# Optimization experiments

Measured on AMD Instinct MI355X. Metric: run time of the kernel, lower is better.

## Reference

```python
import jax, jax.numpy as jnp
import numpy as np

PROJ_DIM = 128
CLASS_NUM = 7
QUEUE_SIZE = 150
TEMP = 0.5
EPS = 1e-8


def _l2norm(x):
    # torch F.normalize(dim=1) with eps clamp
    n = jnp.linalg.norm(x, axis=1, keepdims=True)
    return x / jnp.maximum(n, 1e-12)


def setup_inputs() -> dict:
    key = jax.random.key(0)
    k1, k2, k3, k4 = jax.random.split(key, 4)
    B = 65536
    activation = jax.random.normal(k1, (B, PROJ_DIM), dtype=jnp.float32)
    ema_activation = jax.random.normal(k2, (B, PROJ_DIM), dtype=jnp.float32)
    pseudo_label = jax.random.normal(k3, (B, CLASS_NUM), dtype=jnp.float32)
    queue_list = jax.random.normal(k4, (QUEUE_SIZE * CLASS_NUM, PROJ_DIM), dtype=jnp.float32)
    queue_list = _l2norm(queue_list)  # buffer is row-normalized at init
    return {
        "activation": activation,
        "ema_activation": ema_activation,
        "pseudo_label": pseudo_label,
        "queue_list": queue_list,
    }


def reference(activation, ema_activation, pseudo_label, queue_list):
    f = _l2norm(activation)          # [B, D]
    ema_f = _l2norm(ema_activation)  # [B, D]
    label = jnp.argmax(pseudo_label, axis=1)  # [B]

    # positive pair term: exp(<f_i, ema_f_i>/T)
    l_pos = jnp.exp(jnp.sum(f * ema_f, axis=1) / TEMP)  # [B]

    # similarities against the (snapshotted) queue: [B, C*Qs]
    sim = jnp.exp(jnp.einsum("bd,qd->bq", f, queue_list) / TEMP)

    # denominator = l_pos + pos_sum + neg_sum = l_pos + total_sum over queue
    denom = l_pos + jnp.sum(sim, axis=1)  # [B]

    # which queue rows belong to each sample's pseudo-class
    row_class = jnp.arange(CLASS_NUM * QUEUE_SIZE) // QUEUE_SIZE  # [C*Qs]
    pos_mask = (row_class[None, :] == label[:, None])             # [B, C*Qs]

    # -log(contrast) terms: the ema term plus the QUEUE_SIZE positive terms
    term0 = -jnp.log(l_pos / denom + EPS)                          # [B]
    term1 = -jnp.log(sim / denom[:, None] + EPS)                   # [B, C*Qs]
    pos_terms = jnp.sum(jnp.where(pos_mask, term1, 0.0), axis=1)   # [B]

    per_sample = (term0 + pos_terms) / (QUEUE_SIZE + 1)
    return jnp.mean(per_sample)
```

## Files before the change

kernel.cpp:

```cpp
#include <hip/hip_runtime.h>
#include <stdint.h>

#define CLASS_NUM 7
#define QROWS 1050
#define QPAD  1152
#define NPAD  102
#define NGRP  72
#define GPW   18
#define QSUM_OFF (QPAD * 128)
#define PART_OFF 151552
#define NBLK  1024
#define C2L 2.8853900817779268f
#define USCALE 0x7F7F7F7F

typedef float f32x4 __attribute__((ext_vector_type(4)));
typedef int   i32x8 __attribute__((ext_vector_type(8)));

__device__ __forceinline__ float fexp2(float x) { return __builtin_amdgcn_exp2f(x); }

__device__ __forceinline__ unsigned pk8(float a, float b, float c, float d) {
  int v = __builtin_amdgcn_cvt_pk_fp8_f32(a, b, 0, false);
  v = __builtin_amdgcn_cvt_pk_fp8_f32(c, d, v, true);
  return (unsigned)v;
}

__global__ __launch_bounds__(256) void prep_q8(
    const float* __restrict__ queue, char* __restrict__ ws)
{
  const int b = blockIdx.x, tid = threadIdx.x;
  if (b < NGRP) {
    const int g = b;
    const int lane = tid >> 2, k = tid & 3;
    const int row = g * 16 + (lane & 15);
    const int col = (lane >> 4) * 32 + k * 8;
    uint2 u = {0u, 0u};
    if (row < QROWS) {
      const float4 v0 = *(const float4*)(queue + row * 128 + col);
      const float4 v1 = *(const float4*)(queue + row * 128 + col + 4);
      u.x = pk8(v0.x, v0.y, v0.z, v0.w);
      u.y = pk8(v1.x, v1.y, v1.z, v1.w);
    }
    *(uint2*)(ws + (size_t)g * 2048 + tid * 8) = u;
  } else if (tid < 128) {
    const int c = b - NGRP, d = tid;
    float s = 0.f;
    const float* p = queue + c * 150 * 128 + d;
#pragma unroll 10
    for (int i = 0; i < 150; ++i) s += p[i * 128];
    ((float*)(ws + QSUM_OFF))[c * 128 + d] = s;
  }
}

__global__ __launch_bounds__(256, 2) void pgc_stream(
    const float* __restrict__ act, const float* __restrict__ ema,
    const float* __restrict__ plab, char* __restrict__ ws)
{
  __shared__ __align__(16) char aT[8192];
  __shared__ float s_lpos[64], s_pd[64];
  __shared__ float dnp[4][64];

  const int tid = threadIdx.x, lane = tid & 63, wave = tid >> 6;
  const int lo = lane & 15, hi = lane >> 4;

  {
    const int r = tid >> 2, j4 = tid & 3;
    const long grow = (long)blockIdx.x * 64 + r;
    const float* ap = act + grow * 128 + j4 * 32;
    const float* ep = ema + grow * 128 + j4 * 32;

    float pv0 = plab[grow * CLASS_NUM + j4];
    float pv1 = (j4 + 4 < CLASS_NUM) ? plab[grow * CLASS_NUM + j4 + 4] : -3.4e38f;
    f32x4 a4[8], e4[8];
#pragma unroll
    for (int u = 0; u < 8; ++u) a4[u] = *(const f32x4*)(ap + 4 * u);
#pragma unroll
    for (int u = 0; u < 8; ++u) e4[u] = *(const f32x4*)(ep + 4 * u);

    float a2 = 0.f, e2 = 0.f, ae = 0.f;
#pragma unroll
    for (int u = 0; u < 8; ++u) {
      a2 += a4[u].x*a4[u].x + a4[u].y*a4[u].y + a4[u].z*a4[u].z + a4[u].w*a4[u].w;
      e2 += e4[u].x*e4[u].x + e4[u].y*e4[u].y + e4[u].z*e4[u].z + e4[u].w*e4[u].w;
      ae += a4[u].x*e4[u].x + a4[u].y*e4[u].y + a4[u].z*e4[u].z + a4[u].w*e4[u].w;
    }
#pragma unroll
    for (int m = 1; m < 4; m <<= 1) {
      a2 += __shfl_xor(a2, m);
      e2 += __shfl_xor(e2, m);
      ae += __shfl_xor(ae, m);
    }
    const float rna = rsqrtf(a2), rne = rsqrtf(e2);

    float pv = pv0; int bi = j4;
    if (pv1 > pv0) { pv = pv1; bi = j4 + 4; }
#pragma unroll
    for (int m = 1; m < 4; m <<= 1) {
      const float ov = __shfl_xor(pv, m);
      const int   oi = __shfl_xor(bi, m);
      if (ov > pv || (ov == pv && oi < bi)) { pv = ov; bi = oi; }
    }

    const float* qs = (const float*)(ws + QSUM_OFF) + bi * 128 + j4 * 32;
    float pdot = 0.f;
#pragma unroll
    for (int u = 0; u < 8; ++u) {
      const float4 qv = *(const float4*)(qs + 4 * u);
      pdot += a4[u].x*qv.x + a4[u].y*qv.y + a4[u].z*qv.z + a4[u].w*qv.w;
    }
#pragma unroll
    for (int m = 1; m < 4; m <<= 1) pdot += __shfl_xor(pdot, m);

    if (j4 == 0) {
      s_lpos[r] = ae * rna * rne * C2L;
      s_pd[r]   = pdot * rna;
    }

    const float sc = rna * C2L;
    const int st = r >> 4, tl = j4 * 16 + (r & 15);
    uint4 w0, w1;
    w0.x = pk8(a4[0].x*sc, a4[0].y*sc, a4[0].z*sc, a4[0].w*sc);
    w0.y = pk8(a4[1].x*sc, a4[1].y*sc, a4[1].z*sc, a4[1].w*sc);
    w0.z = pk8(a4[2].x*sc, a4[2].y*sc, a4[2].z*sc, a4[2].w*sc);
    w0.w = pk8(a4[3].x*sc, a4[3].y*sc, a4[3].z*sc, a4[3].w*sc);
    w1.x = pk8(a4[4].x*sc, a4[4].y*sc, a4[4].z*sc, a4[4].w*sc);
    w1.y = pk8(a4[5].x*sc, a4[5].y*sc, a4[5].z*sc, a4[5].w*sc);
    w1.z = pk8(a4[6].x*sc, a4[6].y*sc, a4[6].z*sc, a4[6].w*sc);
    w1.w = pk8(a4[7].x*sc, a4[7].y*sc, a4[7].z*sc, a4[7].w*sc);
    *(uint4*)(aT + st * 2048 + tl * 32)      = w0;
    *(uint4*)(aT + st * 2048 + tl * 32 + 16) = w1;
  }
  __syncthreads();

  i32x8 sa[4];
#pragma unroll
  for (int s = 0; s < 4; ++s)
    sa[s] = *(const i32x8*)(aT + s * 2048 + lane * 32);

  float dn[4][4] = {{0.f,0.f,0.f,0.f},{0.f,0.f,0.f,0.f},
                    {0.f,0.f,0.f,0.f},{0.f,0.f,0.f,0.f}};
  const f32x4 Z = {0.f, 0.f, 0.f, 0.f};
  const char* qp = ws + (size_t)(wave * GPW) * 2048 + (size_t)lane * 32;

  i32x8 B0, B1, B2;
#define LOADG(X, G)  { X = *(const i32x8*)(qp + (G) * 2048); }
#define COMPG(X)                                                        \
  { _Pragma("unroll")                                                   \
    for (int s = 0; s < 4; ++s) {                                       \
      f32x4 c = __builtin_amdgcn_mfma_scale_f32_16x16x128_f8f6f4(       \
          sa[s], X, Z, 0, 0, 0, USCALE, 0, USCALE);                     \
      _Pragma("unroll")                                                 \
      for (int rg = 0; rg < 4; ++rg) dn[s][rg] += fexp2(c[rg]);         \
    } }

  LOADG(B0, 0)
  LOADG(B1, 1)
  LOADG(B2, 2)
#pragma unroll 1
  for (int g = 0; g < GPW - 3; g += 3) {
    COMPG(B0) LOADG(B0, g + 3)
    COMPG(B1) LOADG(B1, g + 4)
    COMPG(B2) LOADG(B2, g + 5)
  }
  COMPG(B0)
  COMPG(B1)
  COMPG(B2)
#undef LOADG
#undef COMPG

#pragma unroll
  for (int s = 0; s < 4; ++s)
#pragma unroll
    for (int rg = 0; rg < 4; ++rg)
#pragma unroll
      for (int m = 1; m < 16; m <<= 1)
        dn[s][rg] += __shfl_xor(dn[s][rg], m);

  if (lo == 0) {
#pragma unroll
    for (int s = 0; s < 4; ++s)
#pragma unroll
      for (int rg = 0; rg < 4; ++rg)
        dnp[wave][s * 16 + hi * 4 + rg] = dn[s][rg];
  }
  __syncthreads();

  if (tid < 64) {
    const int i = tid;
    const float dtot = dnp[0][i] + dnp[1][i] + dnp[2][i] + dnp[3][i];
    const float lp   = exp2f(s_lpos[i]);
    const float dnf  = lp + dtot - (float)NPAD;
    float loss = -logf(lp / dnf + 1e-8f) + 150.0f * logf(dnf) - 2.0f * s_pd[i];
#pragma unroll
    for (int m = 1; m < 64; m <<= 1) loss += __shfl_xor(loss, m);
    if (tid == 0)
      ((float*)(ws + PART_OFF))[blockIdx.x] = loss;
  }
}

__global__ __launch_bounds__(1024) void finalize(
    const char* __restrict__ ws, float* __restrict__ out)
{
  __shared__ float sred[16];
  const int tid = threadIdx.x;
  float v = ((const float*)(ws + PART_OFF))[tid];
#pragma unroll
  for (int m = 1; m < 64; m <<= 1) v += __shfl_xor(v, m);
  if ((tid & 63) == 0) sred[tid >> 6] = v;
  __syncthreads();
  if (tid < 16) {
    float s = sred[tid];
#pragma unroll
    for (int m = 1; m < 16; m <<= 1) s += __shfl_xor(s, m);
    if (tid == 0) *out = s * (1.0f / (151.0f * 65536.0f));
  }
}

extern "C" void kernel_launch(void* const* d_in, const int* in_sizes, int n_in,
                              void* d_out, int out_size, void* d_ws, size_t ws_size,
                              hipStream_t stream) {
  const float* act   = (const float*)d_in[0];
  const float* ema   = (const float*)d_in[1];
  const float* plab  = (const float*)d_in[2];
  const float* queue = (const float*)d_in[3];
  float* out = (float*)d_out;

  prep_q8<<<dim3(NGRP + CLASS_NUM), dim3(256), 0, stream>>>(queue, (char*)d_ws);

  pgc_stream<<<dim3(NBLK), dim3(256), 0, stream>>>(act, ema, plab, (char*)d_ws);

  finalize<<<dim3(1), dim3(1024), 0, stream>>>((const char*)d_ws, out);
}
```

Before: 38.50 us.

## Stage activation and EMA tiles through LDS with direct global-to-LDS loads

```diff
diff --git a/kernel.cpp b/kernel.cpp
--- a/kernel.cpp
+++ b/kernel.cpp
@@ -55,79 +55,72 @@
     const float* __restrict__ act, const float* __restrict__ ema,
     const float* __restrict__ plab, char* __restrict__ ws)
 {
-  __shared__ __align__(16) char aT[8192];
-  __shared__ float s_lpos[64], s_pd[64];
-  __shared__ float dnp[4][64];
+  __shared__ __align__(16) char smem[75520];
+  char*  stage  = smem;
+  char*  aT     = smem + 65536;
+  int*   s_lab  = (int*)  (smem + 73728);
+  float* s_lpos = (float*)(smem + 73984);
+  float* s_pd   = (float*)(smem + 74240);
+  float (*dnp)[64] = (float(*)[64])(smem + 74496);
 
   const int tid = threadIdx.x, lane = tid & 63, wave = tid >> 6;
   const int lo = lane & 15, hi = lane >> 4;
 
   {
-    const int r = tid >> 2, j4 = tid & 3;
-    const long grow = (long)blockIdx.x * 64 + r;
-    const float* ap = act + grow * 128 + j4 * 32;
-    const float* ep = ema + grow * 128 + j4 * 32;
-
-    float pv0 = plab[grow * CLASS_NUM + j4];
-    float pv1 = (j4 + 4 < CLASS_NUM) ? plab[grow * CLASS_NUM + j4 + 4] : -3.4e38f;
-    f32x4 a4[8], e4[8];
-#pragma unroll
-    for (int u = 0; u < 8; ++u) a4[u] = *(const f32x4*)(ap + 4 * u);
-#pragma unroll
-    for (int u = 0; u < 8; ++u) e4[u] = *(const f32x4*)(ep + 4 * u);
-
-    float a2 = 0.f, e2 = 0.f, ae = 0.f;
-#pragma unroll
-    for (int u = 0; u < 8; ++u) {
-      a2 += a4[u].x*a4[u].x + a4[u].y*a4[u].y + a4[u].z*a4[u].z + a4[u].w*a4[u].w;
-      e2 += e4[u].x*e4[u].x + e4[u].y*e4[u].y + e4[u].z*e4[u].z + e4[u].w*e4[u].w;
-      ae += a4[u].x*e4[u].x + a4[u].y*e4[u].y + a4[u].z*e4[u].z + a4[u].w*e4[u].w;
+    const char* actB = (const char*)(act + (size_t)blockIdx.x * 64 * 128);
+    const char* emaB = (const char*)(ema + (size_t)blockIdx.x * 64 * 128);
+    const char* src = (wave < 2) ? actB + wave * 16384 : emaB + (wave - 2) * 16384;
+    char* dst = stage + wave * 16384;
+#pragma unroll
+    for (int i = 0; i < 16; ++i)
+      __builtin_amdgcn_global_load_lds(
+          (const __attribute__((address_space(1))) void*)(src + i * 1024 + lane * 16),
+          (__attribute__((address_space(3))) void*)(dst + i * 1024), 16, 0, 0);
+  }
+
+  if (tid < 64) {
+    const float* pp = plab + ((size_t)blockIdx.x * 64 + tid) * CLASS_NUM;
+    float best = pp[0]; int bi = 0;
+#pragma unroll
+    for (int c = 1; c < CLASS_NUM; ++c) {
+      const float v = pp[c];
+      if (v > best) { best = v; bi = c; }
     }
-#pragma unroll
-    for (int m = 1; m < 4; m <<= 1) {
-      a2 += __shfl_xor(a2, m);
-      e2 += __shfl_xor(e2, m);
-      ae += __shfl_xor(ae, m);
+    s_lab[tid] = bi;
+  }
+  __syncthreads();
+
+  {
+    const int b5 = tid & 31;
+    const int h  = tid >> 5;
+#pragma unroll
+    for (int k = 0; k < 8; ++k) {
+      const int row = h + k * 8;
+      const f32x4 a4 = *(const f32x4*)(stage + tid * 16 + k * 4096);
+      const f32x4 e4 = *(const f32x4*)(stage + 32768 + tid * 16 + k * 4096);
+      const f32x4 q4 = *(const f32x4*)((const float*)(ws + QSUM_OFF) +
+                                       s_lab[row] * 128 + b5 * 4);
+      float a2 = a4.x*a4.x + a4.y*a4.y + a4.z*a4.z + a4.w*a4.w;
+      float e2 = e4.x*e4.x + e4.y*e4.y + e4.z*e4.z + e4.w*e4.w;
+      float ae = a4.x*e4.x + a4.y*e4.y + a4.z*e4.z + a4.w*e4.w;
+      float pd = a4.x*q4.x + a4.y*q4.y + a4.z*q4.z + a4.w*q4.w;
+#pragma unroll
+      for (int m = 1; m < 32; m <<= 1) {
+        a2 += __shfl_xor(a2, m);
+        e2 += __shfl_xor(e2, m);
+        ae += __shfl_xor(ae, m);
+        pd += __shfl_xor(pd, m);
+      }
+      const float rna = rsqrtf(a2), rne = rsqrtf(e2);
+      if (b5 == 0) {
+        s_lpos[row] = ae * rna * rne * C2L;
+        s_pd[row]   = pd * rna;
+      }
+      const float sc = rna * C2L;
+      const int st = row >> 4, tl = (b5 >> 3) * 16 + (row & 15);
+      *(unsigned*)(aT + st * 2048 + tl * 32 + (b5 & 7) * 4) =
+          pk8(a4.x * sc, a4.y * sc, a4.z * sc, a4.w * sc);
     }
-    const float rna = rsqrtf(a2), rne = rsqrtf(e2);
-
-    float pv = pv0; int bi = j4;
-    if (pv1 > pv0) { pv = pv1; bi = j4 + 4; }
-#pragma unroll
-    for (int m = 1; m < 4; m <<= 1) {
-      const float ov = __shfl_xor(pv, m);
-      const int   oi = __shfl_xor(bi, m);
-      if (ov > pv || (ov == pv && oi < bi)) { pv = ov; bi = oi; }
-    }
-
-    const float* qs = (const float*)(ws + QSUM_OFF) + bi * 128 + j4 * 32;
-    float pdot = 0.f;
-#pragma unroll
-    for (int u = 0; u < 8; ++u) {
-      const float4 qv = *(const float4*)(qs + 4 * u);
-      pdot += a4[u].x*qv.x + a4[u].y*qv.y + a4[u].z*qv.z + a4[u].w*qv.w;
-    }
-#pragma unroll
-    for (int m = 1; m < 4; m <<= 1) pdot += __shfl_xor(pdot, m);
-
-    if (j4 == 0) {
-      s_lpos[r] = ae * rna * rne * C2L;
-      s_pd[r]   = pdot * rna;
-    }
-
-    const float sc = rna * C2L;
-    const int st = r >> 4, tl = j4 * 16 + (r & 15);
-    uint4 w0, w1;
-    w0.x = pk8(a4[0].x*sc, a4[0].y*sc, a4[0].z*sc, a4[0].w*sc);
-    w0.y = pk8(a4[1].x*sc, a4[1].y*sc, a4[1].z*sc, a4[1].w*sc);
-    w0.z = pk8(a4[2].x*sc, a4[2].y*sc, a4[2].z*sc, a4[2].w*sc);
-    w0.w = pk8(a4[3].x*sc, a4[3].y*sc, a4[3].z*sc, a4[3].w*sc);
-    w1.x = pk8(a4[4].x*sc, a4[4].y*sc, a4[4].z*sc, a4[4].w*sc);
-    w1.y = pk8(a4[5].x*sc, a4[5].y*sc, a4[5].z*sc, a4[5].w*sc);
-    w1.z = pk8(a4[6].x*sc, a4[6].y*sc, a4[6].z*sc, a4[6].w*sc);
-    w1.w = pk8(a4[7].x*sc, a4[7].y*sc, a4[7].z*sc, a4[7].w*sc);
-    *(uint4*)(aT + st * 2048 + tl * 32)      = w0;
-    *(uint4*)(aT + st * 2048 + tl * 32 + 16) = w1;
   }
   __syncthreads();
 
```

Measured after the change: 42.01 us. 9.1% more time.

## Fuse final reduction into main kernel via last-block atomic and stagger queue reads

Applied to the files above, without the earlier changes.

```diff
diff --git a/kernel.cpp b/kernel.cpp
--- a/kernel.cpp
+++ b/kernel.cpp
@@ -9,6 +9,7 @@
 #define GPW   18
 #define QSUM_OFF (QPAD * 128)
 #define PART_OFF 151552
+#define CNT_OFF  155648
 #define NBLK  1024
 #define C2L 2.8853900817779268f
 #define USCALE 0x7F7F7F7F
@@ -28,6 +29,7 @@
     const float* __restrict__ queue, char* __restrict__ ws)
 {
   const int b = blockIdx.x, tid = threadIdx.x;
+  if (b == 0 && tid == 0) *(unsigned*)(ws + CNT_OFF) = 0u;
   if (b < NGRP) {
     const int g = b;
     const int lane = tid >> 2, k = tid & 3;
@@ -53,11 +55,13 @@
 
 __global__ __launch_bounds__(256, 2) void pgc_stream(
     const float* __restrict__ act, const float* __restrict__ ema,
-    const float* __restrict__ plab, char* __restrict__ ws)
+    const float* __restrict__ plab, char* __restrict__ ws,
+    float* __restrict__ out)
 {
   __shared__ __align__(16) char aT[8192];
   __shared__ float s_lpos[64], s_pd[64];
   __shared__ float dnp[4][64];
+  __shared__ int s_last;
 
   const int tid = threadIdx.x, lane = tid & 63, wave = tid >> 6;
   const int lo = lane & 15, hi = lane >> 4;
@@ -140,9 +144,12 @@
                     {0.f,0.f,0.f,0.f},{0.f,0.f,0.f,0.f}};
   const f32x4 Z = {0.f, 0.f, 0.f, 0.f};
   const char* qp = ws + (size_t)(wave * GPW) * 2048 + (size_t)lane * 32;
+  const int base = blockIdx.x % GPW;
 
   i32x8 B0, B1, B2;
-#define LOADG(X, G)  { X = *(const i32x8*)(qp + (G) * 2048); }
+#define LOADG(X, G)                                                     \
+  { int gi_ = (G) + base; if (gi_ >= GPW) gi_ -= GPW;                   \
+    X = *(const i32x8*)(qp + gi_ * 2048); }
 #define COMPG(X)                                                        \
   { _Pragma("unroll")                                                   \
     for (int s = 0; s < 4; ++s) {                                       \
@@ -195,23 +202,24 @@
     if (tid == 0)
       ((float*)(ws + PART_OFF))[blockIdx.x] = loss;
   }
-}
-
-__global__ __launch_bounds__(1024) void finalize(
-    const char* __restrict__ ws, float* __restrict__ out)
-{
-  __shared__ float sred[16];
-  const int tid = threadIdx.x;
-  float v = ((const float*)(ws + PART_OFF))[tid];
-#pragma unroll
-  for (int m = 1; m < 64; m <<= 1) v += __shfl_xor(v, m);
-  if ((tid & 63) == 0) sred[tid >> 6] = v;
+
+  __threadfence();
+  if (tid == 0) {
+    const unsigned old = atomicAdd((unsigned*)(ws + CNT_OFF), 1u);
+    s_last = (old == NBLK - 1u) ? 1 : 0;
+  }
   __syncthreads();
-  if (tid < 16) {
-    float s = sred[tid];
-#pragma unroll
-    for (int m = 1; m < 16; m <<= 1) s += __shfl_xor(s, m);
-    if (tid == 0) *out = s * (1.0f / (151.0f * 65536.0f));
+  if (s_last) {
+    __threadfence();
+    const float* parts = (const float*)(ws + PART_OFF);
+    float v = parts[tid] + parts[tid + 256] + parts[tid + 512] + parts[tid + 768];
+#pragma unroll
+    for (int m = 1; m < 64; m <<= 1) v += __shfl_xor(v, m);
+    if (lane == 0) dnp[0][wave] = v;
+    __syncthreads();
+    if (tid == 0)
+      *out = (dnp[0][0] + dnp[0][1] + dnp[0][2] + dnp[0][3]) *
+             (1.0f / (151.0f * 65536.0f));
   }
 }
 
@@ -226,7 +234,6 @@
 
   prep_q8<<<dim3(NGRP + CLASS_NUM), dim3(256), 0, stream>>>(queue, (char*)d_ws);
 
-  pgc_stream<<<dim3(NBLK), dim3(256), 0, stream>>>(act, ema, plab, (char*)d_ws);
-
-  finalize<<<dim3(1), dim3(1024), 0, stream>>>((const char*)d_ws, out);
-}
+  pgc_stream<<<dim3(NBLK), dim3(256), 0, stream>>>(
+      act, ema, plab, (char*)d_ws, out);
+}
```

Result: slower. 98.35 us (+155.4%).
